# Optimization experiments

Measured on AMD Instinct MI355X. Metric: run time of the kernel, lower is better.

Reference implementation:

```python
import jax, jax.numpy as jnp
import numpy as np

N_NODES = 100000
N_EDGES = 1600000
IN_DIM = 128
OUT_DIM = 32
HEADS = 4
NEG_SLOPE = 0.2  # PyG GATConv default
EPS = 1e-16      # PyG softmax denom eps


def setup_inputs() -> dict:
    key = jax.random.key(0)
    ks = jax.random.split(key, 8)
    x = jax.random.normal(ks[0], (N_NODES, IN_DIM), dtype=jnp.float32)
    edge_index = jax.random.randint(ks[1], (2, N_EDGES), 0, N_NODES, dtype=jnp.int64)
    # GATConv params: lin (no bias), att_src/att_dst, output bias; then LayerNorm
    glorot = 1.0 / np.sqrt(IN_DIM)
    W = jax.random.uniform(ks[2], (IN_DIM, HEADS * OUT_DIM), dtype=jnp.float32,
                           minval=-glorot, maxval=glorot)
    ga = 1.0 / np.sqrt(OUT_DIM)
    att_src = jax.random.uniform(ks[3], (1, HEADS, OUT_DIM), dtype=jnp.float32, minval=-ga, maxval=ga)
    att_dst = jax.random.uniform(ks[4], (1, HEADS, OUT_DIM), dtype=jnp.float32, minval=-ga, maxval=ga)
    bias = jnp.zeros((HEADS * OUT_DIM,), dtype=jnp.float32)
    gamma = jnp.ones((HEADS * OUT_DIM,), dtype=jnp.float32)
    beta = jnp.zeros((HEADS * OUT_DIM,), dtype=jnp.float32)
    return {"x": x, "edge_index": edge_index, "W": W, "att_src": att_src,
            "att_dst": att_dst, "bias": bias, "gamma": gamma, "beta": beta}


def _gat_layer(x, edge_index, W, att_src, att_dst, bias, gamma, beta):
    N = x.shape[0]
    H, C = att_src.shape[1], att_src.shape[2]
    # add self loops (PyG default add_self_loops=True)
    loop = jnp.arange(N, dtype=edge_index.dtype)
    src = jnp.concatenate([edge_index[0], loop])
    dst = jnp.concatenate([edge_index[1], loop])

    h = (x @ W).reshape(N, H, C)                       # [N,H,C]
    a_src = jnp.sum(h * att_src, axis=-1)               # [N,H]
    a_dst = jnp.sum(h * att_dst, axis=-1)               # [N,H]

    logits = a_src[src] + a_dst[dst]                    # [E,H]
    logits = jnp.where(logits > 0, logits, NEG_SLOPE * logits)  # leaky_relu

    # segment softmax grouped by destination node
    seg_max = jax.ops.segment_max(logits, dst, num_segments=N)  # [N,H]
    e = jnp.exp(logits - seg_max[dst])
    denom = jax.ops.segment_sum(e, dst, num_segments=N)         # [N,H]
    alpha = e / (denom[dst] + EPS)                               # [E,H]

    msgs = h[src] * alpha[:, :, None]                    # [E,H,C]
    out = jax.ops.segment_sum(msgs, dst, num_segments=N) # [N,H,C]
    out = out.reshape(N, H * C) + bias                   # concat=True

    # LayerNorm + ReLU (dropout is identity in eval)
    mu = jnp.mean(out, axis=-1, keepdims=True)
    var = jnp.var(out, axis=-1, keepdims=True)
    out = (out - mu) * jax.lax.rsqrt(var + 1e-5) * gamma + beta
    return jax.nn.relu(out)


def reference(x, edge_index, W, att_src, att_dst, bias, gamma, beta):
    return _gat_layer(x, edge_index, W, att_src, att_dst, bias, gamma, beta)
```

## Files before the change

kernel.cpp:

```cpp
#include <hip/hip_runtime.h>

#define N_NODES 100000
#define N_EDGES 1600000
#define IN_DIM 128
#define ODIM 128
#define HEADS 4
#define NEG_SLOPE 0.2f
#define NTILES 782

__device__ __forceinline__ float lrelu(float v) { return v > 0.f ? v : NEG_SLOPE * v; }

__global__ __launch_bounds__(512) void k1_gemm_att(
    const float* __restrict__ x, const float* __restrict__ W,
    const float* __restrict__ att_src, const float* __restrict__ att_dst,
    float* __restrict__ h, float* __restrict__ asrc, float* __restrict__ adst)
{
    extern __shared__ float lds[];
    float* Wl = lds;
    float* xT = lds + 128 * 128;
    const int t = threadIdx.x;

    for (int j = 0; j < 8; ++j) {
        int idx = t + j * 512;
        int k = idx >> 5, c4 = idx & 31;
        *(float4*)(Wl + k * 128 + c4 * 4) = ((const float4*)W)[idx];
    }

    const int cg = t & 15;
    const int rg = t >> 4;
    const int c0 = cg * 8;
    const int head = cg >> 2, q = cg & 3;
    const float4 aS0 = *(const float4*)(att_src + c0);
    const float4 aS1 = *(const float4*)(att_src + c0 + 4);
    const float4 aD0 = *(const float4*)(att_dst + c0);
    const float4 aD1 = *(const float4*)(att_dst + c0 + 4);

    for (int tile = blockIdx.x; tile < NTILES; tile += gridDim.x) {
        __syncthreads();
        for (int j = 0; j < 8; ++j) {
            int idx = t + j * 512;
            int row = idx >> 5, k0 = (idx & 31) * 4;
            int grow = tile * 128 + row;
            float4 xv = make_float4(0.f, 0.f, 0.f, 0.f);
            if (grow < N_NODES) xv = *(const float4*)(x + (size_t)grow * IN_DIM + k0);
            #pragma unroll
            for (int i = 0; i < 4; ++i) {
                int k = k0 + i;
                int sw = ((k >> 2) & 7) << 2;
                xT[k * 136 + (row ^ sw)] = (&xv.x)[i];
            }
        }
        __syncthreads();

        float acc[4][8];
        #pragma unroll
        for (int r = 0; r < 4; ++r)
            #pragma unroll
            for (int j = 0; j < 8; ++j) acc[r][j] = 0.f;

        const int r0 = rg * 4;
        #pragma unroll 4
        for (int k = 0; k < 128; ++k) {
            int sw = ((k >> 2) & 7) << 2;
            const float4 xa = *(const float4*)(xT + k * 136 + (r0 ^ sw));
            const float4 w0 = *(const float4*)(Wl + k * 128 + c0);
            const float4 w1 = *(const float4*)(Wl + k * 128 + c0 + 4);
            #pragma unroll
            for (int r = 0; r < 4; ++r) {
                float xr = (&xa.x)[r];
                acc[r][0] = fmaf(xr, w0.x, acc[r][0]);
                acc[r][1] = fmaf(xr, w0.y, acc[r][1]);
                acc[r][2] = fmaf(xr, w0.z, acc[r][2]);
                acc[r][3] = fmaf(xr, w0.w, acc[r][3]);
                acc[r][4] = fmaf(xr, w1.x, acc[r][4]);
                acc[r][5] = fmaf(xr, w1.y, acc[r][5]);
                acc[r][6] = fmaf(xr, w1.z, acc[r][6]);
                acc[r][7] = fmaf(xr, w1.w, acc[r][7]);
            }
        }

        #pragma unroll
        for (int r = 0; r < 4; ++r) {
            int grow = tile * 128 + r0 + r;
            bool ok = grow < N_NODES;
            float4 lo = make_float4(acc[r][0], acc[r][1], acc[r][2], acc[r][3]);
            float4 hi = make_float4(acc[r][4], acc[r][5], acc[r][6], acc[r][7]);
            if (ok) {
                *(float4*)(h + (size_t)grow * ODIM + c0)     = lo;
                *(float4*)(h + (size_t)grow * ODIM + c0 + 4) = hi;
            }
            float pS = lo.x*aS0.x + lo.y*aS0.y + lo.z*aS0.z + lo.w*aS0.w
                     + hi.x*aS1.x + hi.y*aS1.y + hi.z*aS1.z + hi.w*aS1.w;
            float pD = lo.x*aD0.x + lo.y*aD0.y + lo.z*aD0.z + lo.w*aD0.w
                     + hi.x*aD1.x + hi.y*aD1.y + hi.z*aD1.z + hi.w*aD1.w;
            pS += __shfl_xor(pS, 1); pS += __shfl_xor(pS, 2);
            pD += __shfl_xor(pD, 1); pD += __shfl_xor(pD, 2);
            if (ok && q == 0) {
                asrc[grow * HEADS + head] = pS;
                adst[grow * HEADS + head] = pD;
            }
        }
    }
}

__global__ __launch_bounds__(256) void k2_count(const int* __restrict__ ei,
                                                int* __restrict__ count)
{
    int e = blockIdx.x * 256 + threadIdx.x;
    if (e >= N_EDGES) return;
    int dst = ei[N_EDGES + e];
    atomicAdd(&count[dst], 1);
}

__global__ __launch_bounds__(256) void k3_alloc(const int* __restrict__ count,
                                                int* __restrict__ cur,
                                                int* __restrict__ cursor)
{
    int n = blockIdx.x * 256 + threadIdx.x;
    if (n >= N_NODES) return;
    int s = atomicAdd(cursor, count[n]);
    cur[n] = s;
}

__global__ __launch_bounds__(256) void k4_scatter(const int* __restrict__ ei,
                                                  int* __restrict__ cur,
                                                  int* __restrict__ esrc)
{
    int e = blockIdx.x * 256 + threadIdx.x;
    if (e >= N_EDGES) return;
    int src = ei[e];
    int dst = ei[N_EDGES + e];
    int pos = atomicAdd(&cur[dst], 1);
    esrc[pos] = src;
}

__global__ __launch_bounds__(256) void k5_aggregate(
    const float* __restrict__ h, const float* __restrict__ asrc, const float* __restrict__ adst,
    const int* __restrict__ cur, const int* __restrict__ count,
    const int* __restrict__ esrc,
    const float* __restrict__ bias, const float* __restrict__ gamma, const float* __restrict__ beta,
    float* __restrict__ out)
{
    const int wid = (blockIdx.x * blockDim.x + threadIdx.x) >> 6;
    if (wid >= N_NODES) return;
    const int lane = threadIdx.x & 63;
    const int n = wid;
    const int c = count[n];
    const int s = cur[n] - c;

    const float4 aDn = *(const float4*)(adst + (size_t)n * HEADS);

    float4 aSn = *(const float4*)(asrc + (size_t)n * HEADS);
    float4 sl;
    sl.x = lrelu(aSn.x + aDn.x); sl.y = lrelu(aSn.y + aDn.y);
    sl.z = lrelu(aSn.z + aDn.z); sl.w = lrelu(aSn.w + aDn.w);

    float4 mx = sl;
    float4 sm = {0,0,0,0};
    for (int e = lane; e < c; e += 64) {
        int sn = esrc[s + e];
        float4 a1 = *(const float4*)(asrc + (size_t)sn * HEADS);
        float lgx = lrelu(a1.x + aDn.x), lgy = lrelu(a1.y + aDn.y);
        float lgz = lrelu(a1.z + aDn.z), lgw = lrelu(a1.w + aDn.w);
        float nmx = fmaxf(mx.x, lgx), nmy = fmaxf(mx.y, lgy);
        float nmz = fmaxf(mx.z, lgz), nmw = fmaxf(mx.w, lgw);
        sm.x = sm.x * __expf(mx.x - nmx) + __expf(lgx - nmx);
        sm.y = sm.y * __expf(mx.y - nmy) + __expf(lgy - nmy);
        sm.z = sm.z * __expf(mx.z - nmz) + __expf(lgz - nmz);
        sm.w = sm.w * __expf(mx.w - nmw) + __expf(lgw - nmw);
        mx.x = nmx; mx.y = nmy; mx.z = nmz; mx.w = nmw;
    }
    #pragma unroll
    for (int m = 1; m < 64; m <<= 1) {
        float omx = __shfl_xor(mx.x, m), osx = __shfl_xor(sm.x, m);
        float omy = __shfl_xor(mx.y, m), osy = __shfl_xor(sm.y, m);
        float omz = __shfl_xor(mx.z, m), osz = __shfl_xor(sm.z, m);
        float omw = __shfl_xor(mx.w, m), osw = __shfl_xor(sm.w, m);
        float nmx = fmaxf(mx.x, omx), nmy = fmaxf(mx.y, omy);
        float nmz = fmaxf(mx.z, omz), nmw = fmaxf(mx.w, omw);
        sm.x = sm.x * __expf(mx.x - nmx) + osx * __expf(omx - nmx);
        sm.y = sm.y * __expf(mx.y - nmy) + osy * __expf(omy - nmy);
        sm.z = sm.z * __expf(mx.z - nmz) + osz * __expf(omz - nmz);
        sm.w = sm.w * __expf(mx.w - nmw) + osw * __expf(omw - nmw);
        mx.x = nmx; mx.y = nmy; mx.z = nmz; mx.w = nmw;
    }
    float4 den;
    den.x = sm.x + __expf(sl.x - mx.x) + 1e-16f;
    den.y = sm.y + __expf(sl.y - mx.y) + 1e-16f;
    den.z = sm.z + __expf(sl.z - mx.z) + 1e-16f;
    den.w = sm.w + __expf(sl.w - mx.w) + 1e-16f;

    const int half = lane >> 5, li = lane & 31;
    const int col0 = li * 4, hg = li >> 3;
    float mh   = hg == 0 ? mx.x  : hg == 1 ? mx.y  : hg == 2 ? mx.z  : mx.w;
    float dh   = hg == 0 ? den.x : hg == 1 ? den.y : hg == 2 ? den.z : den.w;
    float slh  = hg == 0 ? sl.x  : hg == 1 ? sl.y  : hg == 2 ? sl.z  : sl.w;
    float aDh  = hg == 0 ? aDn.x : hg == 1 ? aDn.y : hg == 2 ? aDn.z : aDn.w;
    float invh = 1.0f / dh;

    float4 acc = {0,0,0,0};
    for (int e = half; e < c; e += 2) {
        int sn = esrc[s + e];
        float as_ = asrc[(size_t)sn * HEADS + hg];
        float w = __expf(lrelu(as_ + aDh) - mh) * invh;
        const float4 hv = *(const float4*)(h + (size_t)sn * ODIM + col0);
        acc.x = fmaf(hv.x, w, acc.x); acc.y = fmaf(hv.y, w, acc.y);
        acc.z = fmaf(hv.z, w, acc.z); acc.w = fmaf(hv.w, w, acc.w);
    }
    if (half == 0) {
        float w = __expf(slh - mh) * invh;
        const float4 hv = *(const float4*)(h + (size_t)n * ODIM + col0);
        acc.x = fmaf(hv.x, w, acc.x); acc.y = fmaf(hv.y, w, acc.y);
        acc.z = fmaf(hv.z, w, acc.z); acc.w = fmaf(hv.w, w, acc.w);
    }
    acc.x += __shfl_xor(acc.x, 32); acc.y += __shfl_xor(acc.y, 32);
    acc.z += __shfl_xor(acc.z, 32); acc.w += __shfl_xor(acc.w, 32);

    const float4 b4 = *(const float4*)(bias + col0);
    acc.x += b4.x; acc.y += b4.y; acc.z += b4.z; acc.w += b4.w;
    float ss = acc.x + acc.y + acc.z + acc.w;
    float sq = acc.x*acc.x + acc.y*acc.y + acc.z*acc.z + acc.w*acc.w;
    #pragma unroll
    for (int m = 1; m < 32; m <<= 1) {
        ss += __shfl_xor(ss, m); sq += __shfl_xor(sq, m);
    }
    float mean = ss * (1.0f / 128.0f);
    float var  = sq * (1.0f / 128.0f) - mean * mean;
    float rstd = rsqrtf(var + 1e-5f);
    const float4 g4 = *(const float4*)(gamma + col0);
    const float4 e4 = *(const float4*)(beta + col0);
    float4 o;
    o.x = fmaxf((acc.x - mean) * rstd * g4.x + e4.x, 0.f);
    o.y = fmaxf((acc.y - mean) * rstd * g4.y + e4.y, 0.f);
    o.z = fmaxf((acc.z - mean) * rstd * g4.z + e4.z, 0.f);
    o.w = fmaxf((acc.w - mean) * rstd * g4.w + e4.w, 0.f);
    if (half == 0) *(float4*)(out + (size_t)n * ODIM + col0) = o;
}

extern "C" void kernel_launch(void* const* d_in, const int* in_sizes, int n_in,
                              void* d_out, int out_size, void* d_ws, size_t ws_size,
                              hipStream_t stream)
{
    const float* x       = (const float*)d_in[0];
    const int*   ei      = (const int*)d_in[1];
    const float* W       = (const float*)d_in[2];
    const float* att_src = (const float*)d_in[3];
    const float* att_dst = (const float*)d_in[4];
    const float* bias    = (const float*)d_in[5];
    const float* gamma   = (const float*)d_in[6];
    const float* beta    = (const float*)d_in[7];
    float* out = (float*)d_out;

    char* ws = (char*)d_ws;
    size_t off = 0;
    auto alloc = [&](size_t bytes) -> void* {
        void* p = ws + off;
        off += (bytes + 511) & ~(size_t)511;
        return p;
    };
    float* h      = (float*)alloc((size_t)N_NODES * ODIM * 4);
    float* asrc   = (float*)alloc((size_t)N_NODES * HEADS * 4);
    float* adst   = (float*)alloc((size_t)N_NODES * HEADS * 4);
    int*   count  = (int*)  alloc((size_t)N_NODES * 4 + 4);
    int*   cursor = count + N_NODES;
    int*   cur    = (int*)  alloc((size_t)N_NODES * 4);
    int*   esrc   = (int*)  alloc((size_t)N_EDGES * 4);

    hipMemsetAsync(count, 0, (size_t)N_NODES * 4 + 4, stream);

    const int k1_lds = (128 * 128 + 128 * 136) * 4;
    hipFuncSetAttribute((const void*)k1_gemm_att,
                        hipFuncAttributeMaxDynamicSharedMemorySize, k1_lds);

    k1_gemm_att<<<256, 512, k1_lds, stream>>>(x, W, att_src, att_dst, h, asrc, adst);
    k2_count<<<N_EDGES / 256, 256, 0, stream>>>(ei, count);
    k3_alloc<<<(N_NODES + 255) / 256, 256, 0, stream>>>(count, cur, cursor);
    k4_scatter<<<N_EDGES / 256, 256, 0, stream>>>(ei, cur, esrc);
    k5_aggregate<<<(N_NODES * 64 + 255) / 256, 256, 0, stream>>>(
        h, asrc, adst, cur, count, esrc, bias, gamma, beta, out);
}
```

Baseline: 531.1 us.

## Fuse edge counting into GEMM, read x directly, batch scatter and gather loads

The GEMM kernel drops its transposed x tile in LDS and reads x rows straight from global memory, keeping only W in static LDS. That frees shared memory, so the grid doubles to 512 blocks. The degree-count kernel is folded into the tail of the GEMM kernel, which removes one launch. The scatter kernel now handles four edges per thread to overlap the index loads and atomics, and the aggregation loop is unrolled four-way to keep more gathers in flight. The risks are uncoalesced global x loads in the GEMM and extra register pressure from the unrolling.

```diff
diff --git a/kernel.cpp b/kernel.cpp
--- a/kernel.cpp
+++ b/kernel.cpp
@@ -13,18 +13,17 @@
 __global__ __launch_bounds__(512) void k1_gemm_att(
     const float* __restrict__ x, const float* __restrict__ W,
     const float* __restrict__ att_src, const float* __restrict__ att_dst,
-    float* __restrict__ h, float* __restrict__ asrc, float* __restrict__ adst)
-{
-    extern __shared__ float lds[];
-    float* Wl = lds;
-    float* xT = lds + 128 * 128;
+    float* __restrict__ h, float* __restrict__ asrc, float* __restrict__ adst,
+    const int* __restrict__ ei, int* __restrict__ count)
+{
+    __shared__ float Wl[128 * 128];
     const int t = threadIdx.x;
 
     for (int j = 0; j < 8; ++j) {
         int idx = t + j * 512;
-        int k = idx >> 5, c4 = idx & 31;
-        *(float4*)(Wl + k * 128 + c4 * 4) = ((const float4*)W)[idx];
-    }
+        ((float4*)Wl)[idx] = ((const float4*)W)[idx];
+    }
+    __syncthreads();
 
     const int cg = t & 15;
     const int rg = t >> 4;
@@ -36,21 +35,15 @@
     const float4 aD1 = *(const float4*)(att_dst + c0 + 4);
 
     for (int tile = blockIdx.x; tile < NTILES; tile += gridDim.x) {
-        __syncthreads();
-        for (int j = 0; j < 8; ++j) {
-            int idx = t + j * 512;
-            int row = idx >> 5, k0 = (idx & 31) * 4;
-            int grow = tile * 128 + row;
-            float4 xv = make_float4(0.f, 0.f, 0.f, 0.f);
-            if (grow < N_NODES) xv = *(const float4*)(x + (size_t)grow * IN_DIM + k0);
-            #pragma unroll
-            for (int i = 0; i < 4; ++i) {
-                int k = k0 + i;
-                int sw = ((k >> 2) & 7) << 2;
-                xT[k * 136 + (row ^ sw)] = (&xv.x)[i];
-            }
+        const int r0 = tile * 128 + rg * 4;
+        const float* xr[4];
+        bool okr[4];
+        #pragma unroll
+        for (int r = 0; r < 4; ++r) {
+            int gr = r0 + r;
+            okr[r] = gr < N_NODES;
+            xr[r] = x + (size_t)(okr[r] ? gr : 0) * IN_DIM;
         }
-        __syncthreads();
 
         float acc[4][8];
         #pragma unroll
@@ -58,34 +51,36 @@
             #pragma unroll
             for (int j = 0; j < 8; ++j) acc[r][j] = 0.f;
 
-        const int r0 = rg * 4;
-        #pragma unroll 4
-        for (int k = 0; k < 128; ++k) {
-            int sw = ((k >> 2) & 7) << 2;
-            const float4 xa = *(const float4*)(xT + k * 136 + (r0 ^ sw));
-            const float4 w0 = *(const float4*)(Wl + k * 128 + c0);
-            const float4 w1 = *(const float4*)(Wl + k * 128 + c0 + 4);
+        #pragma unroll 2
+        for (int k = 0; k < 128; k += 4) {
+            float4 xv[4];
             #pragma unroll
-            for (int r = 0; r < 4; ++r) {
-                float xr = (&xa.x)[r];
-                acc[r][0] = fmaf(xr, w0.x, acc[r][0]);
-                acc[r][1] = fmaf(xr, w0.y, acc[r][1]);
-                acc[r][2] = fmaf(xr, w0.z, acc[r][2]);
-                acc[r][3] = fmaf(xr, w0.w, acc[r][3]);
-                acc[r][4] = fmaf(xr, w1.x, acc[r][4]);
-                acc[r][5] = fmaf(xr, w1.y, acc[r][5]);
-                acc[r][6] = fmaf(xr, w1.z, acc[r][6]);
-                acc[r][7] = fmaf(xr, w1.w, acc[r][7]);
+            for (int r = 0; r < 4; ++r) xv[r] = *(const float4*)(xr[r] + k);
+            #pragma unroll
+            for (int kk = 0; kk < 4; ++kk) {
+                const float4 w0 = *(const float4*)(Wl + (k + kk) * 128 + c0);
+                const float4 w1 = *(const float4*)(Wl + (k + kk) * 128 + c0 + 4);
+                #pragma unroll
+                for (int r = 0; r < 4; ++r) {
+                    float xs = (&xv[r].x)[kk];
+                    acc[r][0] = fmaf(xs, w0.x, acc[r][0]);
+                    acc[r][1] = fmaf(xs, w0.y, acc[r][1]);
+                    acc[r][2] = fmaf(xs, w0.z, acc[r][2]);
+                    acc[r][3] = fmaf(xs, w0.w, acc[r][3]);
+                    acc[r][4] = fmaf(xs, w1.x, acc[r][4]);
+                    acc[r][5] = fmaf(xs, w1.y, acc[r][5]);
+                    acc[r][6] = fmaf(xs, w1.z, acc[r][6]);
+                    acc[r][7] = fmaf(xs, w1.w, acc[r][7]);
+                }
             }
         }
 
         #pragma unroll
         for (int r = 0; r < 4; ++r) {
-            int grow = tile * 128 + r0 + r;
-            bool ok = grow < N_NODES;
+            int grow = r0 + r;
             float4 lo = make_float4(acc[r][0], acc[r][1], acc[r][2], acc[r][3]);
             float4 hi = make_float4(acc[r][4], acc[r][5], acc[r][6], acc[r][7]);
-            if (ok) {
+            if (okr[r]) {
                 *(float4*)(h + (size_t)grow * ODIM + c0)     = lo;
                 *(float4*)(h + (size_t)grow * ODIM + c0 + 4) = hi;
             }
@@ -95,21 +90,17 @@
                      + hi.x*aD1.x + hi.y*aD1.y + hi.z*aD1.z + hi.w*aD1.w;
             pS += __shfl_xor(pS, 1); pS += __shfl_xor(pS, 2);
             pD += __shfl_xor(pD, 1); pD += __shfl_xor(pD, 2);
-            if (ok && q == 0) {
+            if (okr[r] && q == 0) {
                 asrc[grow * HEADS + head] = pS;
                 adst[grow * HEADS + head] = pD;
             }
         }
     }
-}
-
-__global__ __launch_bounds__(256) void k2_count(const int* __restrict__ ei,
-                                                int* __restrict__ count)
-{
-    int e = blockIdx.x * 256 + threadIdx.x;
-    if (e >= N_EDGES) return;
-    int dst = ei[N_EDGES + e];
-    atomicAdd(&count[dst], 1);
+
+    const int stride = gridDim.x * 512;
+    for (int e = blockIdx.x * 512 + t; e < N_EDGES; e += stride) {
+        atomicAdd(&count[ei[N_EDGES + e]], 1);
+    }
 }
 
 __global__ __launch_bounds__(256) void k3_alloc(const int* __restrict__ count,
@@ -126,12 +117,23 @@
                                                   int* __restrict__ cur,
                                                   int* __restrict__ esrc)
 {
-    int e = blockIdx.x * 256 + threadIdx.x;
-    if (e >= N_EDGES) return;
-    int src = ei[e];
-    int dst = ei[N_EDGES + e];
-    int pos = atomicAdd(&cur[dst], 1);
-    esrc[pos] = src;
+    const int tid = blockIdx.x * 256 + threadIdx.x;
+    const int stride = gridDim.x * 256;
+    int e0 = tid, e1 = tid + stride, e2 = tid + 2 * stride, e3 = tid + 3 * stride;
+    int s0, s1, s2, s3, d0, d1, d2, d3;
+    if (e0 < N_EDGES) { s0 = ei[e0]; d0 = ei[N_EDGES + e0]; }
+    if (e1 < N_EDGES) { s1 = ei[e1]; d1 = ei[N_EDGES + e1]; }
+    if (e2 < N_EDGES) { s2 = ei[e2]; d2 = ei[N_EDGES + e2]; }
+    if (e3 < N_EDGES) { s3 = ei[e3]; d3 = ei[N_EDGES + e3]; }
+    int p0, p1, p2, p3;
+    if (e0 < N_EDGES) p0 = atomicAdd(&cur[d0], 1);
+    if (e1 < N_EDGES) p1 = atomicAdd(&cur[d1], 1);
+    if (e2 < N_EDGES) p2 = atomicAdd(&cur[d2], 1);
+    if (e3 < N_EDGES) p3 = atomicAdd(&cur[d3], 1);
+    if (e0 < N_EDGES) esrc[p0] = s0;
+    if (e1 < N_EDGES) esrc[p1] = s1;
+    if (e2 < N_EDGES) esrc[p2] = s2;
+    if (e3 < N_EDGES) esrc[p3] = s3;
 }
 
 __global__ __launch_bounds__(256) void k5_aggregate(
@@ -149,7 +151,6 @@
     const int s = cur[n] - c;
 
     const float4 aDn = *(const float4*)(adst + (size_t)n * HEADS);
-
     float4 aSn = *(const float4*)(asrc + (size_t)n * HEADS);
     float4 sl;
     sl.x = lrelu(aSn.x + aDn.x); sl.y = lrelu(aSn.y + aDn.y);
@@ -199,7 +200,30 @@
     float invh = 1.0f / dh;
 
     float4 acc = {0,0,0,0};
-    for (int e = half; e < c; e += 2) {
+    int e = half;
+    for (; e + 6 < c; e += 8) {
+        int sn0 = esrc[s + e],     sn1 = esrc[s + e + 2];
+        int sn2 = esrc[s + e + 4], sn3 = esrc[s + e + 6];
+        float a0 = asrc[(size_t)sn0 * HEADS + hg], a1 = asrc[(size_t)sn1 * HEADS + hg];
+        float a2 = asrc[(size_t)sn2 * HEADS + hg], a3 = asrc[(size_t)sn3 * HEADS + hg];
+        const float4 h0 = *(const float4*)(h + (size_t)sn0 * ODIM + col0);
+        const float4 h1 = *(const float4*)(h + (size_t)sn1 * ODIM + col0);
+        const float4 h2 = *(const float4*)(h + (size_t)sn2 * ODIM + col0);
+        const float4 h3 = *(const float4*)(h + (size_t)sn3 * ODIM + col0);
+        float w0 = __expf(lrelu(a0 + aDh) - mh) * invh;
+        float w1 = __expf(lrelu(a1 + aDh) - mh) * invh;
+        float w2 = __expf(lrelu(a2 + aDh) - mh) * invh;
+        float w3 = __expf(lrelu(a3 + aDh) - mh) * invh;
+        acc.x = fmaf(h0.x, w0, acc.x); acc.y = fmaf(h0.y, w0, acc.y);
+        acc.z = fmaf(h0.z, w0, acc.z); acc.w = fmaf(h0.w, w0, acc.w);
+        acc.x = fmaf(h1.x, w1, acc.x); acc.y = fmaf(h1.y, w1, acc.y);
+        acc.z = fmaf(h1.z, w1, acc.z); acc.w = fmaf(h1.w, w1, acc.w);
+        acc.x = fmaf(h2.x, w2, acc.x); acc.y = fmaf(h2.y, w2, acc.y);
+        acc.z = fmaf(h2.z, w2, acc.z); acc.w = fmaf(h2.w, w2, acc.w);
+        acc.x = fmaf(h3.x, w3, acc.x); acc.y = fmaf(h3.y, w3, acc.y);
+        acc.z = fmaf(h3.z, w3, acc.z); acc.w = fmaf(h3.w, w3, acc.w);
+    }
+    for (; e < c; e += 2) {
         int sn = esrc[s + e];
         float as_ = asrc[(size_t)sn * HEADS + hg];
         float w = __expf(lrelu(as_ + aDh) - mh) * invh;
@@ -268,14 +292,9 @@
 
     hipMemsetAsync(count, 0, (size_t)N_NODES * 4 + 4, stream);
 
-    const int k1_lds = (128 * 128 + 128 * 136) * 4;
-    hipFuncSetAttribute((const void*)k1_gemm_att,
-                        hipFuncAttributeMaxDynamicSharedMemorySize, k1_lds);
-
-    k1_gemm_att<<<256, 512, k1_lds, stream>>>(x, W, att_src, att_dst, h, asrc, adst);
-    k2_count<<<N_EDGES / 256, 256, 0, stream>>>(ei, count);
+    k1_gemm_att<<<512, 512, 0, stream>>>(x, W, att_src, att_dst, h, asrc, adst, ei, count);
     k3_alloc<<<(N_NODES + 255) / 256, 256, 0, stream>>>(count, cur, cursor);
-    k4_scatter<<<N_EDGES / 256, 256, 0, stream>>>(ei, cur, esrc);
+    k4_scatter<<<(N_EDGES + 1023) / 1024, 256, 0, stream>>>(ei, cur, esrc);
     k5_aggregate<<<(N_NODES * 64 + 255) / 256, 256, 0, stream>>>(
         h, asrc, adst, cur, count, esrc, bias, gamma, beta, out);
 }
```

Result: faster. 467.2 us (-12.0%).
